# Kernel optimization log

Measured on AMD Instinct MI355X. Metric: run time of the kernel, lower is better.

## Reference

```python
import jax, jax.numpy as jnp
import numpy as np

N_NODES = 50000
N_EDGES = 800000
D_NODE = 128
D_EDGE = 128
D_HID = 128
D_OUT = 128


def setup_inputs() -> dict:
    key = jax.random.key(0)
    ks = jax.random.split(key, 6)
    d_in = 2 * D_NODE + D_EDGE  # 384
    return {
        "cell_attr": jax.random.normal(ks[0], (N_NODES, D_NODE), dtype=jnp.float32),
        "edge_attr": jax.random.normal(ks[1], (N_EDGES, D_EDGE), dtype=jnp.float32),
        "W1": jax.random.normal(ks[2], (d_in, D_HID), dtype=jnp.float32) * (1.0 / np.sqrt(d_in)),
        "b1": jnp.zeros((D_HID,), dtype=jnp.float32),
        "W2": jax.random.normal(ks[3], (D_HID, D_OUT), dtype=jnp.float32) * (1.0 / np.sqrt(D_HID)),
        "b2": jnp.zeros((D_OUT,), dtype=jnp.float32),
        "edge_index": jax.random.randint(ks[4], (2, N_EDGES), 0, N_NODES, dtype=jnp.int64) if jax.config.jax_enable_x64 else jax.random.randint(ks[4], (2, N_EDGES), 0, N_NODES, dtype=jnp.int32),
    }


def reference(cell_attr, edge_attr, W1, b1, W2, b2, edge_index):
    # Gather sender/receiver node features via edge_index: [E, d_node] each
    senders_attr = cell_attr[edge_index[0]]
    receivers_attr = cell_attr[edge_index[1]]
    # Concat -> [E, 2*d_node + d_edge]
    collected = jnp.concatenate([senders_attr, receivers_attr, edge_attr], axis=1)
    # MLP (custom_func): Linear -> ReLU -> Linear
    h = jax.nn.relu(collected @ W1 + b1)
    edge_attr_new = h @ W2 + b2
    return edge_attr_new
```

## Files before the change

### kernel.cpp

```cpp
#include <hip/hip_runtime.h>
#include <stdint.h>

#define D 128
#define K1 384
#define TM 128
#define N_EDGES 800000
#define N_NODES 50000

typedef __attribute__((ext_vector_type(8))) short short8;
typedef __attribute__((ext_vector_type(4))) float f32x4;
typedef unsigned int u32;

__device__ __forceinline__ u32 bf16_rne(float f) {
    u32 u = __builtin_bit_cast(u32, f);
    return (u + 0x7FFFu + ((u >> 16) & 1u)) >> 16;
}
__device__ __forceinline__ u32 pk2(float lo, float hi) {
    return bf16_rne(lo) | (bf16_rne(hi) << 16);
}

__device__ __forceinline__ void gl_lds16(const void* g, void* l) {
    __builtin_amdgcn_global_load_lds(
        (const __attribute__((address_space(1))) void*)g,
        (__attribute__((address_space(3))) void*)l,
        16, 0, 0);
}

__global__ void prep_cell(const float* __restrict__ src, unsigned short* __restrict__ dst, int n4) {
    int i = blockIdx.x * blockDim.x + threadIdx.x;
    if (i >= n4) return;
    float4 v = ((const float4*)src)[i];
    ushort4 o;
    o.x = (unsigned short)bf16_rne(v.x);
    o.y = (unsigned short)bf16_rne(v.y);
    o.z = (unsigned short)bf16_rne(v.z);
    o.w = (unsigned short)bf16_rne(v.w);
    ((ushort4*)dst)[i] = o;
}

__global__ void prep_w(const float* __restrict__ W1, const float* __restrict__ W2,
                       unsigned short* __restrict__ W1F, unsigned short* __restrict__ W2F) {
    int id = blockIdx.x * blockDim.x + threadIdx.x;
    if (id < K1 * D) {
        int k = id >> 7, n = id & 127;
        int c = k >> 7, kr = k & 127;
        int kk = kr >> 5, q = (kr >> 3) & 3, e = kr & 7;
        int wn = n >> 6, nt = (n >> 4) & 3, l16 = n & 15;
        int seg = (((c * 4 + kk) * 2 + wn) * 4 + nt) * 64 + q * 16 + l16;
        W1F[seg * 8 + e] = (unsigned short)bf16_rne(W1[id]);
    } else {
        int id2 = id - K1 * D;
        int k = id2 >> 7, n = id2 & 127;
        int kk = k >> 5, q = (k >> 3) & 3, e = k & 7;
        int wn = n >> 6, nt = (n >> 4) & 3, l16 = n & 15;
        int seg = ((kk * 2 + wn) * 4 + nt) * 64 + q * 16 + l16;
        W2F[seg * 8 + e] = (unsigned short)bf16_rne(W2[id2]);
    }
}

template <bool CELL_BF16>
__global__ __launch_bounds__(256, 2) void edge_mlp(
    const float* __restrict__ cell_f32,
    const unsigned short* __restrict__ cellb,
    const float* __restrict__ edge_attr,
    const unsigned short* __restrict__ W1F,
    const float* __restrict__ b1,
    const unsigned short* __restrict__ W2F,
    const float* __restrict__ b2,
    const int* __restrict__ sidx,
    const int* __restrict__ ridx,
    float* __restrict__ out)
{
    __shared__ __align__(16) unsigned short sA[TM * D];

    const int tid  = threadIdx.x;
    const int lane = tid & 63;
    const int wave = tid >> 6;
    const int l16  = lane & 15;
    const int q    = lane >> 4;
    const int wm   = wave >> 1;
    const int wn   = wave & 1;
    const int e0   = blockIdx.x * TM;
    const int seg  = tid & 15;
    const int rb   = tid >> 4;

    auto stage_cell = [&](const int* __restrict__ idxp) {
        if constexpr (CELL_BF16) {
            const int srcoff = (seg ^ (rb & 7)) * 8;
            char* ldst = (char*)sA + wave * 1024;
#pragma unroll
            for (int it = 0; it < 8; ++it) {
                const int node = idxp[e0 + rb + it * 16];
                gl_lds16(cellb + (size_t)node * D + srcoff, ldst + it * 4096);
            }
        } else {
            const int doff = (seg ^ (rb & 7)) * 16;
#pragma unroll
            for (int it = 0; it < 8; ++it) {
                const int row = rb + it * 16;
                const int node = idxp[e0 + row];
                const float* src = cell_f32 + (size_t)node * D + seg * 8;
                float4 f0 = *(const float4*)src;
                float4 f1 = *(const float4*)(src + 4);
                uint4 v = make_uint4(pk2(f0.x, f0.y), pk2(f0.z, f0.w),
                                     pk2(f1.x, f1.y), pk2(f1.z, f1.w));
                *(uint4*)((char*)sA + row * 256 + doff) = v;
            }
        }
    };

    short8 af[4][4];
    auto read_frags = [&]() {
#pragma unroll
        for (int mt = 0; mt < 4; ++mt) {
            const int row = wm * 64 + mt * 16 + l16;
            const char* rp = (const char*)sA + row * 256;
            const int x = row & 7;
#pragma unroll
            for (int kk = 0; kk < 4; ++kk)
                af[mt][kk] = *(const short8*)(rp + (((kk * 4 + q) ^ x) * 16));
        }
    };

    f32x4 acc[4][4];
#pragma unroll
    for (int i = 0; i < 4; ++i)
#pragma unroll
        for (int j = 0; j < 4; ++j) acc[i][j] = (f32x4){0.f, 0.f, 0.f, 0.f};

    auto compute_chunk = [&](int c) {
#pragma unroll
        for (int kk = 0; kk < 4; ++kk) {
            short8 wf[4];
#pragma unroll
            for (int nt = 0; nt < 4; ++nt)
                wf[nt] = *(const short8*)(W1F + (size_t)((((c * 4 + kk) * 2 + wn) * 4 + nt) * 64 + lane) * 8);
#pragma unroll
            for (int nt = 0; nt < 4; ++nt)
#pragma unroll
                for (int mt = 0; mt < 4; ++mt)
                    acc[nt][mt] = __builtin_amdgcn_mfma_f32_16x16x32_bf16(wf[nt], af[mt][kk], acc[nt][mt], 0, 0, 0);
        }
    };

    stage_cell(sidx);
    __syncthreads();
    read_frags();
    __syncthreads();

    stage_cell(ridx);
    compute_chunk(0);
    __syncthreads();

    read_frags();
    __syncthreads();

    float4 ef0[8], ef1[8];
#pragma unroll
    for (int it = 0; it < 8; ++it) {
        const float* src = edge_attr + (size_t)(e0 + rb + it * 16) * D + seg * 8;
        ef0[it] = *(const float4*)src;
        ef1[it] = *(const float4*)(src + 4);
    }
    compute_chunk(1);
    {
        const int doff = (seg ^ (rb & 7)) * 16;
#pragma unroll
        for (int it = 0; it < 8; ++it) {
            const int row = rb + it * 16;
            uint4 v = make_uint4(pk2(ef0[it].x, ef0[it].y), pk2(ef0[it].z, ef0[it].w),
                                 pk2(ef1[it].x, ef1[it].y), pk2(ef1[it].z, ef1[it].w));
            *(uint4*)((char*)sA + row * 256 + doff) = v;
        }
    }
    __syncthreads();

    read_frags();
    __syncthreads();
    compute_chunk(2);

    f32x4 b1v[4];
#pragma unroll
    for (int nt = 0; nt < 4; ++nt)
        b1v[nt] = *(const f32x4*)(b1 + wn * 64 + nt * 16 + q * 4);

#pragma unroll
    for (int nt = 0; nt < 4; ++nt)
#pragma unroll
        for (int mt = 0; mt < 4; ++mt) {
            f32x4 v = acc[nt][mt] + b1v[nt];
#pragma unroll
            for (int r = 0; r < 4; ++r) v[r] = v[r] > 0.f ? v[r] : 0.f;
            u32 lo = pk2(v[0], v[1]);
            u32 hi = pk2(v[2], v[3]);
            int M = wm * 64 + mt * 16 + l16;
            int slot = (wn * 8 + nt * 2 + (q >> 1)) ^ (M & 7);
            *(uint2*)((char*)sA + M * 256 + slot * 16 + (q & 1) * 8) = make_uint2(lo, hi);
        }
    __syncthreads();

    f32x4 acc2[4][4];
#pragma unroll
    for (int i = 0; i < 4; ++i)
#pragma unroll
        for (int j = 0; j < 4; ++j) acc2[i][j] = (f32x4){0.f, 0.f, 0.f, 0.f};

#pragma unroll
    for (int kk = 0; kk < 4; ++kk) {
        short8 w2f[4], hf[4];
#pragma unroll
        for (int nt = 0; nt < 4; ++nt)
            w2f[nt] = *(const short8*)(W2F + (size_t)(((kk * 2 + wn) * 4 + nt) * 64 + lane) * 8);
#pragma unroll
        for (int mt = 0; mt < 4; ++mt) {
            const int row = wm * 64 + mt * 16 + l16;
            hf[mt] = *(const short8*)((const char*)sA + row * 256 + (((kk * 4 + q) ^ (row & 7)) * 16));
        }
#pragma unroll
        for (int nt = 0; nt < 4; ++nt)
#pragma unroll
            for (int mt = 0; mt < 4; ++mt)
                acc2[nt][mt] = __builtin_amdgcn_mfma_f32_16x16x32_bf16(w2f[nt], hf[mt], acc2[nt][mt], 0, 0, 0);
    }

    f32x4 b2v[4];
#pragma unroll
    for (int nt = 0; nt < 4; ++nt)
        b2v[nt] = *(const f32x4*)(b2 + wn * 64 + nt * 16 + q * 4);

#pragma unroll
    for (int nt = 0; nt < 4; ++nt)
#pragma unroll
        for (int mt = 0; mt < 4; ++mt) {
            f32x4 o = acc2[nt][mt] + b2v[nt];
            *(f32x4*)(out + (size_t)(e0 + wm * 64 + mt * 16 + l16) * D + wn * 64 + nt * 16 + q * 4) = o;
        }
}

extern "C" void kernel_launch(void* const* d_in, const int* in_sizes, int n_in,
                              void* d_out, int out_size, void* d_ws, size_t ws_size,
                              hipStream_t stream) {
    const float* cell = (const float*)d_in[0];
    const float* edge = (const float*)d_in[1];
    const float* W1   = (const float*)d_in[2];
    const float* b1   = (const float*)d_in[3];
    const float* W2   = (const float*)d_in[4];
    const float* b2   = (const float*)d_in[5];
    const int*   eidx = (const int*)d_in[6];

    const size_t cell_bytes = (size_t)N_NODES * D * 2;
    const size_t w1f_bytes  = (size_t)K1 * D * 2;
    const size_t w2f_bytes  = (size_t)D * D * 2;

    bool cell_in_ws = ws_size >= cell_bytes + w1f_bytes + w2f_bytes;
    unsigned short* cellb;
    unsigned short* W1F;
    if (cell_in_ws) {
        cellb = (unsigned short*)d_ws;
        W1F   = (unsigned short*)((char*)d_ws + cell_bytes);
    } else {
        cellb = nullptr;
        W1F   = (unsigned short*)d_ws;
    }
    unsigned short* W2F = W1F + K1 * D;

    if (cell_in_ws) {
        int n4 = N_NODES * D / 4;
        prep_cell<<<(n4 + 255) / 256, 256, 0, stream>>>(cell, cellb, n4);
    }
    prep_w<<<(K1 * D + D * D) / 256, 256, 0, stream>>>(W1, W2, W1F, W2F);

    const int* sidx = eidx;
    const int* ridx = eidx + N_EDGES;
    if (cell_in_ws) {
        edge_mlp<true><<<N_EDGES / TM, 256, 0, stream>>>(
            cell, cellb, edge, W1F, b1, W2F, b2, sidx, ridx, (float*)d_out);
    } else {
        edge_mlp<false><<<N_EDGES / TM, 256, 0, stream>>>(
            cell, cellb, edge, W1F, b1, W2F, b2, sidx, ridx, (float*)d_out);
    }
}
```

Before: 810.2 us.

## Halve edge tile, give each wave all rows, double-buffer LDS, raise occupancy

The edge tile shrinks from 128 to 64 rows. Each of the four waves now computes all 64 rows for a 32-column slice instead of a 64x64 quadrant, and W1 fragments are preloaded per chunk. LDS is split into two 64-row buffers so the receiver gather overlaps the sender chunk's MFMAs, with fewer barriers and no separate fragment-read phase. Launch bounds rise to 4 blocks per SIMD to hide gather latency. In exchange, blocks double, and every block re-reads W1/W2 from global/L2, which adds weight traffic per edge.

Result: faster. 770.0 us (-5.0%).

```diff
diff --git a/kernel.cpp b/kernel.cpp
--- a/kernel.cpp
+++ b/kernel.cpp
@@ -3,7 +3,7 @@
 
 #define D 128
 #define K1 384
-#define TM 128
+#define TM 64
 #define N_EDGES 800000
 #define N_NODES 50000
 
@@ -44,22 +44,22 @@
     if (id < K1 * D) {
         int k = id >> 7, n = id & 127;
         int c = k >> 7, kr = k & 127;
-        int kk = kr >> 5, q = (kr >> 3) & 3, e = kr & 7;
-        int wn = n >> 6, nt = (n >> 4) & 3, l16 = n & 15;
-        int seg = (((c * 4 + kk) * 2 + wn) * 4 + nt) * 64 + q * 16 + l16;
+        int kk = kr >> 5, qq = (kr >> 3) & 3, e = k & 7;
+        int TN = n >> 4, l16 = n & 15;
+        int seg = ((c * 4 + kk) * 8 + TN) * 64 + qq * 16 + l16;
         W1F[seg * 8 + e] = (unsigned short)bf16_rne(W1[id]);
     } else {
         int id2 = id - K1 * D;
         int k = id2 >> 7, n = id2 & 127;
-        int kk = k >> 5, q = (k >> 3) & 3, e = k & 7;
-        int wn = n >> 6, nt = (n >> 4) & 3, l16 = n & 15;
-        int seg = ((kk * 2 + wn) * 4 + nt) * 64 + q * 16 + l16;
+        int kk = k >> 5, qq = (k >> 3) & 3, e = k & 7;
+        int TN = n >> 4, l16 = n & 15;
+        int seg = (kk * 8 + TN) * 64 + qq * 16 + l16;
         W2F[seg * 8 + e] = (unsigned short)bf16_rne(W2[id2]);
     }
 }
 
 template <bool CELL_BF16>
-__global__ __launch_bounds__(256, 2) void edge_mlp(
+__global__ __launch_bounds__(256, 4) void edge_mlp(
     const float* __restrict__ cell_f32,
     const unsigned short* __restrict__ cellb,
     const float* __restrict__ edge_attr,
@@ -71,32 +71,30 @@
     const int* __restrict__ ridx,
     float* __restrict__ out)
 {
-    __shared__ __align__(16) unsigned short sA[TM * D];
+    __shared__ __align__(16) unsigned short sA[2][TM * D];
 
     const int tid  = threadIdx.x;
     const int lane = tid & 63;
     const int wave = tid >> 6;
     const int l16  = lane & 15;
     const int q    = lane >> 4;
-    const int wm   = wave >> 1;
-    const int wn   = wave & 1;
     const int e0   = blockIdx.x * TM;
+    const int rb   = tid >> 4;
     const int seg  = tid & 15;
-    const int rb   = tid >> 4;
-
-    auto stage_cell = [&](const int* __restrict__ idxp) {
+
+    auto stage_cell = [&](const int* __restrict__ idxp, unsigned short* buf) {
         if constexpr (CELL_BF16) {
-            const int srcoff = (seg ^ (rb & 7)) * 8;
-            char* ldst = (char*)sA + wave * 1024;
-#pragma unroll
-            for (int it = 0; it < 8; ++it) {
-                const int node = idxp[e0 + rb + it * 16];
-                gl_lds16(cellb + (size_t)node * D + srcoff, ldst + it * 4096);
+#pragma unroll
+            for (int it = 0; it < 4; ++it) {
+                const int row = it * 16 + wave * 4 + q;
+                const int node = idxp[e0 + row];
+                const int srcoff = (l16 ^ (row & 7)) * 8;
+                gl_lds16(cellb + (size_t)node * D + srcoff,
+                         (char*)buf + wave * 1024 + it * 4096);
             }
         } else {
-            const int doff = (seg ^ (rb & 7)) * 16;
-#pragma unroll
-            for (int it = 0; it < 8; ++it) {
+#pragma unroll
+            for (int it = 0; it < 4; ++it) {
                 const int row = rb + it * 16;
                 const int node = idxp[e0 + row];
                 const float* src = cell_f32 + (size_t)node * D + seg * 8;
@@ -104,136 +102,124 @@
                 float4 f1 = *(const float4*)(src + 4);
                 uint4 v = make_uint4(pk2(f0.x, f0.y), pk2(f0.z, f0.w),
                                      pk2(f1.x, f1.y), pk2(f1.z, f1.w));
-                *(uint4*)((char*)sA + row * 256 + doff) = v;
+                *(uint4*)((char*)buf + row * 256 + ((seg ^ (row & 7)) * 16)) = v;
             }
         }
     };
 
-    short8 af[4][4];
-    auto read_frags = [&]() {
-#pragma unroll
-        for (int mt = 0; mt < 4; ++mt) {
-            const int row = wm * 64 + mt * 16 + l16;
-            const char* rp = (const char*)sA + row * 256;
-            const int x = row & 7;
-#pragma unroll
-            for (int kk = 0; kk < 4; ++kk)
-                af[mt][kk] = *(const short8*)(rp + (((kk * 4 + q) ^ x) * 16));
-        }
+    short8 wf[4][2];
+    auto load_w1 = [&](int c) {
+#pragma unroll
+        for (int kk = 0; kk < 4; ++kk)
+#pragma unroll
+            for (int nt = 0; nt < 2; ++nt)
+                wf[kk][nt] = *(const short8*)(W1F +
+                    (size_t)(((c * 4 + kk) * 8 + wave * 2 + nt) * 64 + lane) * 8);
     };
 
-    f32x4 acc[4][4];
+    f32x4 acc[4][2];
 #pragma unroll
     for (int i = 0; i < 4; ++i)
 #pragma unroll
-        for (int j = 0; j < 4; ++j) acc[i][j] = (f32x4){0.f, 0.f, 0.f, 0.f};
-
-    auto compute_chunk = [&](int c) {
-#pragma unroll
-        for (int kk = 0; kk < 4; ++kk) {
-            short8 wf[4];
-#pragma unroll
-            for (int nt = 0; nt < 4; ++nt)
-                wf[nt] = *(const short8*)(W1F + (size_t)((((c * 4 + kk) * 2 + wn) * 4 + nt) * 64 + lane) * 8);
-#pragma unroll
-            for (int nt = 0; nt < 4; ++nt)
-#pragma unroll
-                for (int mt = 0; mt < 4; ++mt)
-                    acc[nt][mt] = __builtin_amdgcn_mfma_f32_16x16x32_bf16(wf[nt], af[mt][kk], acc[nt][mt], 0, 0, 0);
-        }
+        for (int j = 0; j < 2; ++j) acc[i][j] = (f32x4){0.f, 0.f, 0.f, 0.f};
+
+    auto compute_chunk = [&](const unsigned short* buf) {
+#pragma unroll
+        for (int kk = 0; kk < 4; ++kk)
+#pragma unroll
+            for (int mt = 0; mt < 4; ++mt) {
+                const int row = mt * 16 + l16;
+                short8 a = *(const short8*)((const char*)buf + row * 256 +
+                                            (((kk * 4 + q) ^ (row & 7)) * 16));
+                acc[mt][0] = __builtin_amdgcn_mfma_f32_16x16x32_bf16(wf[kk][0], a, acc[mt][0], 0, 0, 0);
+                acc[mt][1] = __builtin_amdgcn_mfma_f32_16x16x32_bf16(wf[kk][1], a, acc[mt][1], 0, 0, 0);
+            }
     };
 
-    stage_cell(sidx);
-    __syncthreads();
-    read_frags();
-    __syncthreads();
-
-    stage_cell(ridx);
-    compute_chunk(0);
-    __syncthreads();
-
-    read_frags();
-    __syncthreads();
-
-    float4 ef0[8], ef1[8];
-#pragma unroll
-    for (int it = 0; it < 8; ++it) {
+    stage_cell(sidx, sA[0]);
+    __syncthreads();
+
+    load_w1(0);
+    stage_cell(ridx, sA[1]);
+    compute_chunk(sA[0]);
+    __syncthreads();
+
+    load_w1(1);
+    float4 ef0[4], ef1[4];
+#pragma unroll
+    for (int it = 0; it < 4; ++it) {
         const float* src = edge_attr + (size_t)(e0 + rb + it * 16) * D + seg * 8;
         ef0[it] = *(const float4*)src;
         ef1[it] = *(const float4*)(src + 4);
     }
-    compute_chunk(1);
-    {
-        const int doff = (seg ^ (rb & 7)) * 16;
-#pragma unroll
-        for (int it = 0; it < 8; ++it) {
-            const int row = rb + it * 16;
-            uint4 v = make_uint4(pk2(ef0[it].x, ef0[it].y), pk2(ef0[it].z, ef0[it].w),
-                                 pk2(ef1[it].x, ef1[it].y), pk2(ef1[it].z, ef1[it].w));
-            *(uint4*)((char*)sA + row * 256 + doff) = v;
-        }
-    }
-    __syncthreads();
-
-    read_frags();
-    __syncthreads();
-    compute_chunk(2);
-
-    f32x4 b1v[4];
-#pragma unroll
-    for (int nt = 0; nt < 4; ++nt)
-        b1v[nt] = *(const f32x4*)(b1 + wn * 64 + nt * 16 + q * 4);
-
-#pragma unroll
-    for (int nt = 0; nt < 4; ++nt)
+    compute_chunk(sA[1]);
+#pragma unroll
+    for (int it = 0; it < 4; ++it) {
+        const int row = rb + it * 16;
+        uint4 v = make_uint4(pk2(ef0[it].x, ef0[it].y), pk2(ef0[it].z, ef0[it].w),
+                             pk2(ef1[it].x, ef1[it].y), pk2(ef1[it].z, ef1[it].w));
+        *(uint4*)((char*)sA[0] + row * 256 + ((seg ^ (row & 7)) * 16)) = v;
+    }
+    __syncthreads();
+
+    load_w1(2);
+    compute_chunk(sA[0]);
+
+    short8 w2f[4][2];
+#pragma unroll
+    for (int kk = 0; kk < 4; ++kk)
+#pragma unroll
+        for (int nt = 0; nt < 2; ++nt)
+            w2f[kk][nt] = *(const short8*)(W2F +
+                (size_t)((kk * 8 + wave * 2 + nt) * 64 + lane) * 8);
+
+    f32x4 b1v[2];
+#pragma unroll
+    for (int nt = 0; nt < 2; ++nt)
+        b1v[nt] = *(const f32x4*)(b1 + wave * 32 + nt * 16 + q * 4);
+
+#pragma unroll
+    for (int mt = 0; mt < 4; ++mt)
+#pragma unroll
+        for (int nt = 0; nt < 2; ++nt) {
+            f32x4 v = acc[mt][nt] + b1v[nt];
+#pragma unroll
+            for (int r = 0; r < 4; ++r) v[r] = v[r] > 0.f ? v[r] : 0.f;
+            const int M = mt * 16 + l16;
+            const int slot = (wave * 4 + nt * 2 + (q >> 1)) ^ (M & 7);
+            *(uint2*)((char*)sA[1] + M * 256 + slot * 16 + (q & 1) * 8) =
+                make_uint2(pk2(v[0], v[1]), pk2(v[2], v[3]));
+        }
+    __syncthreads();
+
+    f32x4 acc2[4][2];
+#pragma unroll
+    for (int i = 0; i < 4; ++i)
+#pragma unroll
+        for (int j = 0; j < 2; ++j) acc2[i][j] = (f32x4){0.f, 0.f, 0.f, 0.f};
+
+#pragma unroll
+    for (int kk = 0; kk < 4; ++kk)
 #pragma unroll
         for (int mt = 0; mt < 4; ++mt) {
-            f32x4 v = acc[nt][mt] + b1v[nt];
-#pragma unroll
-            for (int r = 0; r < 4; ++r) v[r] = v[r] > 0.f ? v[r] : 0.f;
-            u32 lo = pk2(v[0], v[1]);
-            u32 hi = pk2(v[2], v[3]);
-            int M = wm * 64 + mt * 16 + l16;
-            int slot = (wn * 8 + nt * 2 + (q >> 1)) ^ (M & 7);
-            *(uint2*)((char*)sA + M * 256 + slot * 16 + (q & 1) * 8) = make_uint2(lo, hi);
-        }
-    __syncthreads();
-
-    f32x4 acc2[4][4];
-#pragma unroll
-    for (int i = 0; i < 4; ++i)
-#pragma unroll
-        for (int j = 0; j < 4; ++j) acc2[i][j] = (f32x4){0.f, 0.f, 0.f, 0.f};
-
-#pragma unroll
-    for (int kk = 0; kk < 4; ++kk) {
-        short8 w2f[4], hf[4];
-#pragma unroll
-        for (int nt = 0; nt < 4; ++nt)
-            w2f[nt] = *(const short8*)(W2F + (size_t)(((kk * 2 + wn) * 4 + nt) * 64 + lane) * 8);
-#pragma unroll
-        for (int mt = 0; mt < 4; ++mt) {
-            const int row = wm * 64 + mt * 16 + l16;
-            hf[mt] = *(const short8*)((const char*)sA + row * 256 + (((kk * 4 + q) ^ (row & 7)) * 16));
-        }
-#pragma unroll
-        for (int nt = 0; nt < 4; ++nt)
-#pragma unroll
-            for (int mt = 0; mt < 4; ++mt)
-                acc2[nt][mt] = __builtin_amdgcn_mfma_f32_16x16x32_bf16(w2f[nt], hf[mt], acc2[nt][mt], 0, 0, 0);
-    }
-
-    f32x4 b2v[4];
-#pragma unroll
-    for (int nt = 0; nt < 4; ++nt)
-        b2v[nt] = *(const f32x4*)(b2 + wn * 64 + nt * 16 + q * 4);
-
-#pragma unroll
-    for (int nt = 0; nt < 4; ++nt)
-#pragma unroll
-        for (int mt = 0; mt < 4; ++mt) {
-            f32x4 o = acc2[nt][mt] + b2v[nt];
-            *(f32x4*)(out + (size_t)(e0 + wm * 64 + mt * 16 + l16) * D + wn * 64 + nt * 16 + q * 4) = o;
+            const int row = mt * 16 + l16;
+            short8 h = *(const short8*)((const char*)sA[1] + row * 256 +
+                                        (((kk * 4 + q) ^ (row & 7)) * 16));
+            acc2[mt][0] = __builtin_amdgcn_mfma_f32_16x16x32_bf16(w2f[kk][0], h, acc2[mt][0], 0, 0, 0);
+            acc2[mt][1] = __builtin_amdgcn_mfma_f32_16x16x32_bf16(w2f[kk][1], h, acc2[mt][1], 0, 0, 0);
+        }
+
+    f32x4 b2v[2];
+#pragma unroll
+    for (int nt = 0; nt < 2; ++nt)
+        b2v[nt] = *(const f32x4*)(b2 + wave * 32 + nt * 16 + q * 4);
+
+#pragma unroll
+    for (int mt = 0; mt < 4; ++mt)
+#pragma unroll
+        for (int nt = 0; nt < 2; ++nt) {
+            f32x4 o = acc2[mt][nt] + b2v[nt];
+            *(f32x4*)(out + (size_t)(e0 + mt * 16 + l16) * D + wave * 32 + nt * 16 + q * 4) = o;
         }
 }
 
```
